# Optimization experiments

Hardware: AMD Instinct MI355X
Metric: run time of the kernel (lower is better)

The kernel has to match this reference:

```python
import jax, jax.numpy as jnp
import numpy as np

G, T, D_IN, D_OUT = 8, 4096, 1024, 4096


def setup_inputs() -> dict:
    key = jax.random.key(0)
    k1, k2, k3 = jax.random.split(key, 3)
    x = jax.random.normal(k1, (T, D_IN), dtype=jnp.float32)
    # cumulative end offsets per group: sorted, last == T (grouped_mm convention)
    cuts = jnp.sort(jax.random.randint(k2, (G - 1,), 0, T, dtype=jnp.int32))
    offs = jnp.concatenate([cuts, jnp.array([T], dtype=jnp.int32)])
    weight = jax.random.normal(k3, (G, D_OUT, D_IN), dtype=jnp.float32) * (D_IN ** -0.5)
    return {"input": x, "grouped_mm_offs": offs, "weight": weight}


def reference(input, grouped_mm_offs, weight):
    # Grouped GEMM: row t (with offs[g-1] <= t < offs[g]) -> input[t] @ weight[g].T
    n_tok = input.shape[0]
    tok = jnp.arange(n_tok)
    gid = jnp.searchsorted(grouped_mm_offs, tok, side="right")  # [T] group id per row
    # Dense all-expert projection [G, T, D_OUT], then select the routed expert per row.
    proj = jnp.einsum("ti,goi->gto", input, weight)
    return proj[gid, tok]  # [T, D_OUT]
```

## Files before the change

kernel.cpp:

```cpp
#include <hip/hip_runtime.h>
#include <hip/hip_bf16.h>

#define NG 8
#define NT 4096
#define DIN 1024
#define DOUT 4096
#define BM 128
#define BN 128
#define BK 64
#define KTILES (DIN / BK)
#define NTILES (DOUT / BN)
#define RTILES (NT / BM + NG)
#define THREADS 512
#define ATILESZ (BM * BK * 2)
#define BTILESZ (BN * BK * 2)

typedef __attribute__((ext_vector_type(4))) float f32x4;
typedef __attribute__((ext_vector_type(8))) short bf16x8;

__device__ __forceinline__ void gld16(const void* g, void* l) {
    __builtin_amdgcn_global_load_lds(
        (const __attribute__((address_space(1))) void*)(g),
        (__attribute__((address_space(3))) void*)(l), 16, 0, 0);
}

__device__ __forceinline__ unsigned long long pack4bf(f32x4 v) {
    union { __hip_bfloat16 h; unsigned short u; } c0, c1, c2, c3;
    c0.h = __float2bfloat16(v[0]);
    c1.h = __float2bfloat16(v[1]);
    c2.h = __float2bfloat16(v[2]);
    c3.h = __float2bfloat16(v[3]);
    return (unsigned long long)c0.u | ((unsigned long long)c1.u << 16) |
           ((unsigned long long)c2.u << 32) | ((unsigned long long)c3.u << 48);
}

__device__ __forceinline__ int swz(int row, int colb) {
    return row * 128 + (colb ^ ((row & 7) << 4));
}

__global__ __launch_bounds__(256)
void cvt_x_kernel(const float* __restrict__ x, short* __restrict__ xb) {
    const int n4 = NT * DIN / 4;
    for (int i = blockIdx.x * blockDim.x + threadIdx.x; i < n4;
         i += gridDim.x * blockDim.x) {
        f32x4 v = ((const f32x4*)x)[i];
        ((unsigned long long*)xb)[i] = pack4bf(v);
    }
}

__global__ __launch_bounds__(THREADS, 2)
void grouped_gemm_bf16(const short* __restrict__ xb,
                       const int* __restrict__ offs,
                       const float* __restrict__ w,
                       float* __restrict__ out) {
    __shared__ char lds[2 * ATILESZ + BTILESZ];
    char* ldsA = lds;
    char* ldsB = lds + 2 * ATILESZ;

    const int rt = blockIdx.y;
    const int n0 = blockIdx.x * BN;
    int row0 = 0, endg = 0, gsel = -1;
    {
        int acc0 = 0, prev = 0;
        for (int g = 0; g < NG; ++g) {
            int e = offs[g];
            int cnt = (e - prev + BM - 1) / BM;
            if (rt < acc0 + cnt) { gsel = g; row0 = prev + (rt - acc0) * BM; endg = e; break; }
            acc0 += cnt; prev = e;
        }
    }
    if (gsel < 0) return;
    const float* wg = w + (size_t)gsel * DOUT * DIN;

    const int tid  = threadIdx.x;
    const int lane = tid & 63;
    const int wid  = tid >> 6;
    const int wr   = wid >> 2;
    const int wc   = wid & 3;
    const int lrow = lane & 15, kgrp = lane >> 4;

    int axoff[2], sbaseA[2];
    #pragma unroll
    for (int i = 0; i < 2; ++i) {
        int stripe = wid + i * 8;
        int r = stripe * 8 + (lane >> 3);
        int cs = (lane & 7) ^ (r & 7);
        int ar = row0 + r; if (ar >= endg) ar = endg - 1;
        axoff[i]  = ar * DIN + cs * 8;
        sbaseA[i] = stripe * 1024;
    }
    const int sr = tid >> 4, sc4 = tid & 15;
    int boff[4];
    #pragma unroll
    for (int i = 0; i < 4; ++i) boff[i] = (n0 + sr + i * 32) * DIN + sc4 * 4;

    f32x4 acc[4][2];
    #pragma unroll
    for (int m = 0; m < 4; ++m)
        #pragma unroll
        for (int n = 0; n < 2; ++n)
            acc[m][n] = (f32x4){0.f, 0.f, 0.f, 0.f};

    f32x4 pB[4];

    #pragma unroll
    for (int i = 0; i < 4; ++i) pB[i] = *(const f32x4*)(wg + boff[i]);
    #pragma unroll
    for (int i = 0; i < 2; ++i) gld16(xb + axoff[i], ldsA + sbaseA[i]);
    #pragma unroll
    for (int i = 0; i < 4; ++i)
        *(unsigned long long*)(ldsB + swz(sr + i * 32, sc4 * 8)) = pack4bf(pB[i]);

    for (int kt = 0; kt < KTILES; ++kt) {
        const int cur = kt & 1;
        const char* lA = ldsA + cur * ATILESZ;

        if (kt + 1 < KTILES) {
            const int k0 = (kt + 1) * BK;
            #pragma unroll
            for (int i = 0; i < 4; ++i) pB[i] = *(const f32x4*)(wg + boff[i] + k0);
            #pragma unroll
            for (int i = 0; i < 2; ++i)
                gld16(xb + axoff[i] + k0, ldsA + (cur ^ 1) * ATILESZ + sbaseA[i]);
            __builtin_amdgcn_sched_barrier(0);
            asm volatile("s_waitcnt vmcnt(6) lgkmcnt(0)" ::: "memory");
        } else {
            __builtin_amdgcn_sched_barrier(0);
            asm volatile("s_waitcnt vmcnt(0) lgkmcnt(0)" ::: "memory");
        }
        __builtin_amdgcn_sched_barrier(0);
        __builtin_amdgcn_s_barrier();
        __builtin_amdgcn_sched_barrier(0);

        __builtin_amdgcn_s_setprio(1);
        #pragma unroll
        for (int kk = 0; kk < 2; ++kk) {
            const int kb = kk * 64 + kgrp * 16;
            bf16x8 af[4], bb[2];
            #pragma unroll
            for (int m = 0; m < 4; ++m) {
                int r = wr * 64 + m * 16 + lrow;
                af[m] = *(const bf16x8*)(lA + r * 128 + (((kb >> 4) ^ (r & 7)) << 4));
            }
            #pragma unroll
            for (int n = 0; n < 2; ++n)
                bb[n] = *(const bf16x8*)(ldsB + swz(wc * 32 + n * 16 + lrow, kb));
            #pragma unroll
            for (int m = 0; m < 4; ++m)
                #pragma unroll
                for (int n = 0; n < 2; ++n)
                    acc[m][n] = __builtin_amdgcn_mfma_f32_16x16x32_bf16(
                        af[m], bb[n], acc[m][n], 0, 0, 0);
        }
        __builtin_amdgcn_s_setprio(0);

        if (kt + 1 < KTILES) {
            __builtin_amdgcn_sched_barrier(0);
            __builtin_amdgcn_s_barrier();
            __builtin_amdgcn_sched_barrier(0);
            #pragma unroll
            for (int i = 0; i < 4; ++i)
                *(unsigned long long*)(ldsB + swz(sr + i * 32, sc4 * 8)) = pack4bf(pB[i]);
        }
    }

    #pragma unroll
    for (int m = 0; m < 4; ++m) {
        #pragma unroll
        for (int j = 0; j < 4; ++j) {
            int row = row0 + wr * 64 + m * 16 + kgrp * 4 + j;
            if (row < endg) {
                #pragma unroll
                for (int n = 0; n < 2; ++n) {
                    int col = n0 + wc * 32 + n * 16 + lrow;
                    out[(size_t)row * DOUT + col] = acc[m][n][j];
                }
            }
        }
    }
}

extern "C" void kernel_launch(void* const* d_in, const int* in_sizes, int n_in,
                              void* d_out, int out_size, void* d_ws, size_t ws_size,
                              hipStream_t stream) {
    const float* x    = (const float*)d_in[0];
    const int*   offs = (const int*)d_in[1];
    const float* w    = (const float*)d_in[2];
    float* out = (float*)d_out;
    short* xb  = (short*)d_ws;

    cvt_x_kernel<<<1024, 256, 0, stream>>>(x, xb);
    dim3 grid(NTILES, RTILES, 1);
    grouped_gemm_bf16<<<grid, THREADS, 0, stream>>>(xb, offs, w, out);
}
```

Baseline: 71.86 us.

## Double the row tile to 256 so each converted weight tile feeds two A tiles

Each block now covers 256 token rows as two 128-row A sub-tiles that share one bf16 B tile in LDS. The fp32 weight load and bf16 conversion are paid once per 256 rows instead of once per 128, which halves redundant weight traffic and conversion work. In exchange there are twice the accumulators and A-tile LDS per block, which may lower occupancy below two blocks per CU. Coarser row tiles also waste more rows at group boundaries and leave fewer blocks in the grid.

```diff
diff --git a/kernel.cpp b/kernel.cpp
--- a/kernel.cpp
+++ b/kernel.cpp
@@ -5,14 +5,14 @@
 #define NT 4096
 #define DIN 1024
 #define DOUT 4096
-#define BM 128
+#define BMP 256
 #define BN 128
 #define BK 64
 #define KTILES (DIN / BK)
 #define NTILES (DOUT / BN)
-#define RTILES (NT / BM + NG)
+#define RTILES (NT / BMP + NG)
 #define THREADS 512
-#define ATILESZ (BM * BK * 2)
+#define ATILESZ (128 * BK * 2)
 #define BTILESZ (BN * BK * 2)
 
 typedef __attribute__((ext_vector_type(4))) float f32x4;
@@ -53,20 +53,21 @@
                        const int* __restrict__ offs,
                        const float* __restrict__ w,
                        float* __restrict__ out) {
-    __shared__ char lds[2 * ATILESZ + BTILESZ];
-    char* ldsA = lds;
-    char* ldsB = lds + 2 * ATILESZ;
+    __shared__ char lds[4 * ATILESZ + BTILESZ];
+    char* ldsA0 = lds;
+    char* ldsA1 = lds + 2 * ATILESZ;
+    char* ldsB  = lds + 4 * ATILESZ;
 
     const int rt = blockIdx.y;
     const int n0 = blockIdx.x * BN;
     int row0 = 0, endg = 0, gsel = -1;
     {
-        int acc0 = 0, prev = 0;
+        int acc_ = 0, prev = 0;
         for (int g = 0; g < NG; ++g) {
             int e = offs[g];
-            int cnt = (e - prev + BM - 1) / BM;
-            if (rt < acc0 + cnt) { gsel = g; row0 = prev + (rt - acc0) * BM; endg = e; break; }
-            acc0 += cnt; prev = e;
+            int cnt = (e - prev + BMP - 1) / BMP;
+            if (rt < acc_ + cnt) { gsel = g; row0 = prev + (rt - acc_) * BMP; endg = e; break; }
+            acc_ += cnt; prev = e;
         }
     }
     if (gsel < 0) return;
@@ -79,14 +80,16 @@
     const int wc   = wid & 3;
     const int lrow = lane & 15, kgrp = lane >> 4;
 
-    int axoff[2], sbaseA[2];
+    int axoff0[2], axoff1[2], sbaseA[2];
     #pragma unroll
     for (int i = 0; i < 2; ++i) {
         int stripe = wid + i * 8;
         int r = stripe * 8 + (lane >> 3);
         int cs = (lane & 7) ^ (r & 7);
-        int ar = row0 + r; if (ar >= endg) ar = endg - 1;
-        axoff[i]  = ar * DIN + cs * 8;
+        int a0 = row0 + r;       if (a0 >= endg) a0 = endg - 1;
+        int a1 = row0 + 128 + r; if (a1 >= endg) a1 = endg - 1;
+        axoff0[i] = a0 * DIN + cs * 8;
+        axoff1[i] = a1 * DIN + cs * 8;
         sbaseA[i] = stripe * 1024;
     }
     const int sr = tid >> 4, sc4 = tid & 15;
@@ -94,26 +97,31 @@
     #pragma unroll
     for (int i = 0; i < 4; ++i) boff[i] = (n0 + sr + i * 32) * DIN + sc4 * 4;
 
-    f32x4 acc[4][2];
+    f32x4 acc0[4][2], acc1[4][2];
     #pragma unroll
     for (int m = 0; m < 4; ++m)
         #pragma unroll
-        for (int n = 0; n < 2; ++n)
-            acc[m][n] = (f32x4){0.f, 0.f, 0.f, 0.f};
+        for (int n = 0; n < 2; ++n) {
+            acc0[m][n] = (f32x4){0.f, 0.f, 0.f, 0.f};
+            acc1[m][n] = (f32x4){0.f, 0.f, 0.f, 0.f};
+        }
 
     f32x4 pB[4];
 
     #pragma unroll
     for (int i = 0; i < 4; ++i) pB[i] = *(const f32x4*)(wg + boff[i]);
     #pragma unroll
-    for (int i = 0; i < 2; ++i) gld16(xb + axoff[i], ldsA + sbaseA[i]);
+    for (int i = 0; i < 2; ++i) gld16(xb + axoff0[i], ldsA0 + sbaseA[i]);
+    #pragma unroll
+    for (int i = 0; i < 2; ++i) gld16(xb + axoff1[i], ldsA1 + sbaseA[i]);
     #pragma unroll
     for (int i = 0; i < 4; ++i)
         *(unsigned long long*)(ldsB + swz(sr + i * 32, sc4 * 8)) = pack4bf(pB[i]);
 
     for (int kt = 0; kt < KTILES; ++kt) {
         const int cur = kt & 1;
-        const char* lA = ldsA + cur * ATILESZ;
+        const char* lA0 = ldsA0 + cur * ATILESZ;
+        const char* lA1 = ldsA1 + cur * ATILESZ;
 
         if (kt + 1 < KTILES) {
             const int k0 = (kt + 1) * BK;
@@ -121,9 +129,12 @@
             for (int i = 0; i < 4; ++i) pB[i] = *(const f32x4*)(wg + boff[i] + k0);
             #pragma unroll
             for (int i = 0; i < 2; ++i)
-                gld16(xb + axoff[i] + k0, ldsA + (cur ^ 1) * ATILESZ + sbaseA[i]);
-            __builtin_amdgcn_sched_barrier(0);
-            asm volatile("s_waitcnt vmcnt(6) lgkmcnt(0)" ::: "memory");
+                gld16(xb + axoff0[i] + k0, ldsA0 + (cur ^ 1) * ATILESZ + sbaseA[i]);
+            #pragma unroll
+            for (int i = 0; i < 2; ++i)
+                gld16(xb + axoff1[i] + k0, ldsA1 + (cur ^ 1) * ATILESZ + sbaseA[i]);
+            __builtin_amdgcn_sched_barrier(0);
+            asm volatile("s_waitcnt vmcnt(8) lgkmcnt(0)" ::: "memory");
         } else {
             __builtin_amdgcn_sched_barrier(0);
             asm volatile("s_waitcnt vmcnt(0) lgkmcnt(0)" ::: "memory");
@@ -136,21 +147,27 @@
         #pragma unroll
         for (int kk = 0; kk < 2; ++kk) {
             const int kb = kk * 64 + kgrp * 16;
-            bf16x8 af[4], bb[2];
+            bf16x8 bb[2];
+            #pragma unroll
+            for (int n = 0; n < 2; ++n)
+                bb[n] = *(const bf16x8*)(ldsB + swz(wc * 32 + n * 16 + lrow, kb));
+            bf16x8 af0[4], af1[4];
             #pragma unroll
             for (int m = 0; m < 4; ++m) {
                 int r = wr * 64 + m * 16 + lrow;
-                af[m] = *(const bf16x8*)(lA + r * 128 + (((kb >> 4) ^ (r & 7)) << 4));
+                int off = r * 128 + (((kb >> 4) ^ (r & 7)) << 4);
+                af0[m] = *(const bf16x8*)(lA0 + off);
+                af1[m] = *(const bf16x8*)(lA1 + off);
             }
-            #pragma unroll
-            for (int n = 0; n < 2; ++n)
-                bb[n] = *(const bf16x8*)(ldsB + swz(wc * 32 + n * 16 + lrow, kb));
             #pragma unroll
             for (int m = 0; m < 4; ++m)
                 #pragma unroll
-                for (int n = 0; n < 2; ++n)
-                    acc[m][n] = __builtin_amdgcn_mfma_f32_16x16x32_bf16(
-                        af[m], bb[n], acc[m][n], 0, 0, 0);
+                for (int n = 0; n < 2; ++n) {
+                    acc0[m][n] = __builtin_amdgcn_mfma_f32_16x16x32_bf16(
+                        af0[m], bb[n], acc0[m][n], 0, 0, 0);
+                    acc1[m][n] = __builtin_amdgcn_mfma_f32_16x16x32_bf16(
+                        af1[m], bb[n], acc1[m][n], 0, 0, 0);
+                }
         }
         __builtin_amdgcn_s_setprio(0);
 
@@ -168,12 +185,20 @@
     for (int m = 0; m < 4; ++m) {
         #pragma unroll
         for (int j = 0; j < 4; ++j) {
-            int row = row0 + wr * 64 + m * 16 + kgrp * 4 + j;
-            if (row < endg) {
+            int r0 = row0 + wr * 64 + m * 16 + kgrp * 4 + j;
+            if (r0 < endg) {
                 #pragma unroll
                 for (int n = 0; n < 2; ++n) {
                     int col = n0 + wc * 32 + n * 16 + lrow;
-                    out[(size_t)row * DOUT + col] = acc[m][n][j];
+                    out[(size_t)r0 * DOUT + col] = acc0[m][n][j];
+                }
+            }
+            int r1 = r0 + 128;
+            if (r1 < endg) {
+                #pragma unroll
+                for (int n = 0; n < 2; ++n) {
+                    int col = n0 + wc * 32 + n * 16 + lrow;
+                    out[(size_t)r1 * DOUT + col] = acc1[m][n][j];
                 }
             }
         }
```

After: 78.37 us. +9.1%, slower.
